# Kernel tuning notes

Measured on AMD Instinct MI355X. Metric: run time of the kernel, lower is better.

## Reference

```python
import jax, jax.numpy as jnp
import numpy as np

# Complete K-ary forest: B trees, depth D levels, BFS node numbering per tree.
B, K, D = 64, 4, 6
V, L = 600, 256
N_PER = (K ** D - 1) // (K - 1)   # 1365 nodes per tree
N = B * N_PER                      # 87360 total nodes


def _schedule():
    """Per-(depth, sibling_index) groups, mirroring the torch decode_train loop
    for a complete K-ary forest. Returns list of (d, s, node_idx, parent_idx)."""
    starts = [(K ** d - 1) // (K - 1) for d in range(D)]  # level offsets within a tree
    tree_off = np.arange(B)[:, None] * N_PER
    groups = []
    for d in range(D):
        for s in (range(1) if d == 0 else range(K)):
            if d == 0:
                p = np.arange(1)                      # root
                par = None
            else:
                p = np.arange(K ** (d - 1)) * K + s   # positions with sib_pos == s
                par = (tree_off + starts[d - 1] + (p // K)[None, :]).reshape(-1)
            idx = (tree_off + starts[d] + p[None, :]).reshape(-1)
            groups.append((d, s, jnp.asarray(idx),
                           None if par is None else jnp.asarray(par)))
    return groups

GROUPS = _schedule()


def _lstm(gx, h, c, W_hh, b_ih, b_hh):
    # torch LSTMCell, gate order i, f, g, o; gx = x @ W_ih^T precomputed.
    gates = gx + b_ih + h @ W_hh.T + b_hh
    i, f, g, o = jnp.split(gates, 4, axis=1)
    c_new = jax.nn.sigmoid(f) * c + jax.nn.sigmoid(i) * jnp.tanh(g)
    return jax.nn.sigmoid(o) * jnp.tanh(c_new), c_new


def setup_inputs() -> dict:
    key = jax.random.key(0)
    ks = jax.random.split(key, 20)
    w = lambda k, shape, s=0.05: jax.random.normal(k, shape, dtype=jnp.float32) * s
    return {
        'z': w(ks[0], (B, L), 1.0),
        'features': jax.random.randint(ks[1], (N,), 0, V),
        'W_ih_p': w(ks[2], (4 * L, V)), 'W_hh_p': w(ks[3], (4 * L, L)),
        'b_ih_p': w(ks[4], (4 * L,)), 'b_hh_p': w(ks[5], (4 * L,)),
        'W_ih_s': w(ks[6], (4 * L, V)), 'W_hh_s': w(ks[7], (4 * L, L)),
        'b_ih_s': w(ks[8], (4 * L,)), 'b_hh_s': w(ks[9], (4 * L,)),
        'U_parent': w(ks[10], (L, L)), 'U_sibling': w(ks[11], (L, L)),
        'W_label': w(ks[12], (V, L)), 'b_label': w(ks[13], (V,)),
        'W_depth': w(ks[14], (1, L)), 'b_depth': w(ks[15], (1,)),
        'W_width': w(ks[16], (1, L)), 'b_width': w(ks[17], (1,)),
        'w_off_p': w(ks[18], (1, 1), 1.0), 'w_off_s': w(ks[19], (1, 1), 1.0),
    }


def reference(z, features, W_ih_p, W_hh_p, b_ih_p, b_hh_p,
              W_ih_s, W_hh_s, b_ih_s, b_hh_s, U_parent, U_sibling,
              W_label, b_label, W_depth, b_depth, W_width, b_width,
              w_off_p, w_off_s):
    h_p = jnp.zeros((N, L), jnp.float32)
    c_p = jnp.zeros((N, L), jnp.float32)
    h_s = jnp.zeros((N, L), jnp.float32)
    c_s = jnp.zeros((N, L), jnp.float32)
    pred_labels = jnp.zeros((N, V), jnp.float32)
    pred_is_parent = jnp.zeros((N,), jnp.float32)
    pred_has_sib = jnp.zeros((N,), jnp.float32)

    for d, s, idx, pidx in GROUPS:
        G = idx.shape[0]
        if d == 0:
            h_par, c_par = z, jnp.zeros((B, L), jnp.float32)
        else:
            h_par, c_par = h_p[pidx], c_p[pidx]
        if s == 0:
            h_prev = jnp.zeros((G, L), jnp.float32)
            c_prev = jnp.zeros((G, L), jnp.float32)
        else:
            h_prev, c_prev = h_s[idx - 1], c_s[idx - 1]
        # group-constant teacher flags for a complete K-ary tree
        is_par = 1.0 if d < D - 1 else 0.0
        has_sib = 1.0 if (d > 0 and s < K - 1) else 0.0

        h_pred = jnp.tanh(h_par @ U_parent.T + h_prev @ U_sibling.T)
        logits = h_pred @ W_label.T + b_label
        p_par = jax.nn.sigmoid(h_pred @ W_depth.T + b_depth)[:, 0]
        p_sib = jax.nn.sigmoid(h_pred @ W_width.T + b_width)[:, 0]
        logp = jax.nn.log_softmax(
            logits + w_off_p[0, 0] * is_par + w_off_s[0, 0] * has_sib, axis=1)

        lab = features[idx]
        gx_p = jnp.take(W_ih_p, lab, axis=1).T  # one-hot @ W_ih^T as a gather
        gx_s = jnp.take(W_ih_s, lab, axis=1).T
        hp_new, cp_new = _lstm(gx_p, h_par, c_par, W_hh_p, b_ih_p, b_hh_p)
        hs_new, cs_new = _lstm(gx_s, h_prev, c_prev, W_hh_s, b_ih_s, b_hh_s)

        h_p = h_p.at[idx].set(hp_new)
        c_p = c_p.at[idx].set(cp_new)
        h_s = h_s.at[idx].set(hs_new)
        c_s = c_s.at[idx].set(cs_new)
        pred_labels = pred_labels.at[idx].set(logp)
        pred_is_parent = pred_is_parent.at[idx].set(p_par)
        pred_has_sib = pred_has_sib.at[idx].set(p_sib)

    # pack [N, V+2]: log-softmax labels, p(is_parent), p(has_sibling)
    return jnp.concatenate(
        [pred_labels, pred_is_parent[:, None], pred_has_sib[:, None]], axis=1)
```

## Files before the change

kernel.cpp:

```cpp
#include <hip/hip_runtime.h>


typedef unsigned short u16;
typedef short bf16x8 __attribute__((ext_vector_type(8)));
typedef float f32x4 __attribute__((ext_vector_type(4)));

#define NPER 1365
#define VDIM 600
#define VD2  602

#define MODE_PPA   0
#define MODE_UPROJ 1
#define MODE_ROOT  2

__device__ __forceinline__ float b2f(u16 h) {
  union { unsigned u; float f; } v; v.u = ((unsigned)h) << 16; return v.f;
}
__device__ __forceinline__ u16 f2bf(float f) {
  union { float f; unsigned u; } v; v.f = f;
  unsigned r = v.u + 0x7fff + ((v.u >> 16) & 1);
  return (u16)(r >> 16);
}
__device__ __forceinline__ float fsigm(float x) {
  return __fdividef(1.f, 1.f + __expf(-x));
}
__device__ __forceinline__ float ftanh(float x) {
  float e = __expf(-2.f * fabsf(x));
  float r = __fdividef(1.f - e, 1.f + e);
  return x < 0.f ? -r : r;
}

__device__ __forceinline__ void ladder(int r, int& off, int& pcs, int& start) {
  if (r < 64)        { off = 0;    pcs = 0; start = 1;   }
  else if (r < 320)  { off = 64;   pcs = 2; start = 5;   }
  else if (r < 1344) { off = 320;  pcs = 4; start = 21;  }
  else if (r < 5440) { off = 1344; pcs = 6; start = 85;  }
  else               { off = 5440; pcs = 8; start = 341; }
}

__global__ void k_pack(
    const float* __restrict__ Upar, const float* __restrict__ Whhp,
    const float* __restrict__ Usib, const float* __restrict__ Whhs,
    const float* __restrict__ z, const float* __restrict__ Wihp,
    const float* __restrict__ Wihs, const float* __restrict__ Wlab,
    const float* __restrict__ Wd, const float* __restrict__ Ww,
    const float* __restrict__ blab, const float* __restrict__ bd,
    const float* __restrict__ bw, const float* __restrict__ bihp,
    const float* __restrict__ bhhp, const float* __restrict__ bihs,
    const float* __restrict__ bhhs,
    u16* __restrict__ UPWHHP, u16* __restrict__ USWHHS, u16* __restrict__ ZBF,
    u16* __restrict__ WIHPT, u16* __restrict__ WIHST, u16* __restrict__ WEXT,
    float* __restrict__ BE, float* __restrict__ BP, float* __restrict__ BS) {
  int i = blockIdx.x * 256 + threadIdx.x;
  if (i < 327680) {
    int r = i >> 8, c = i & 255;
    UPWHHP[i] = f2bf(r < 256 ? Upar[(r << 8) | c] : Whhp[((r - 256) << 8) | c]);
    return;
  }
  i -= 327680;
  if (i < 327680) {
    int r = i >> 8, c = i & 255;
    USWHHS[i] = f2bf(r < 256 ? Usib[(r << 8) | c] : Whhs[((r - 256) << 8) | c]);
    return;
  }
  i -= 327680;
  if (i < 16384) { ZBF[i] = f2bf(z[i]); return; }
  i -= 16384;
  if (i < 614400) {
    int r = i >> 10, c = i & 1023;
    WIHPT[i] = f2bf(Wihp[c * VDIM + r]); return;
  }
  i -= 614400;
  if (i < 614400) {
    int r = i >> 10, c = i & 1023;
    WIHST[i] = f2bf(Wihs[c * VDIM + r]); return;
  }
  i -= 614400;
  if (i < VD2 * 256) {
    int r = i >> 8, c = i & 255;
    float v = (r < VDIM) ? Wlab[r * 256 + c] : ((r == VDIM) ? Wd[c] : Ww[c]);
    WEXT[i] = f2bf(v); return;
  }
  i -= VD2 * 256;
  if (i < VD2) { BE[i] = (i < VDIM) ? blab[i] : ((i == VDIM) ? bd[0] : bw[0]); return; }
  i -= VD2;
  if (i < 1024) { BP[i] = bihp[i] + bhhp[i]; return; }
  i -= 1024;
  if (i < 1024) { BS[i] = bihs[i] + bhhs[i]; return; }
}

__device__ __forceinline__ void dev_dual(
    int tile, int nx, const u16* __restrict__ A, const u16* __restrict__ B,
    int M, int mode, u16* __restrict__ ppa, int ppoff,
    float* __restrict__ uproj, u16* __restrict__ gates,
    u16* __restrict__ hroot) {
  static __shared__ __align__(16) u16 As[128 * 40];
  static __shared__ __align__(16) u16 Bs[128 * 40];
  const int m0 = (tile % nx) * 128, n0 = (tile / nx) * 128;
  const int tid = threadIdx.x;
  const int wave = tid >> 6, lane = tid & 63;
  const int quad = lane >> 4, lr = lane & 15;
  const int wm = (wave >> 1) * 64, wn = (wave & 1) * 64;
  const int srow = tid >> 2;
  const int sch = (tid & 3) << 3;

  f32x4 acc[4][4] = {};
  for (int t = 0; t < 8; ++t) {
    const int kk = t * 32;
    bf16x8 a0 = *(const bf16x8*)(A + (size_t)(m0 + srow) * 256 + kk + sch);
    bf16x8 a1 = *(const bf16x8*)(A + (size_t)(m0 + srow + 64) * 256 + kk + sch);
    bf16x8 b0 = *(const bf16x8*)(B + (size_t)(n0 + srow) * 256 + kk + sch);
    bf16x8 b1 = *(const bf16x8*)(B + (size_t)(n0 + srow + 64) * 256 + kk + sch);
    __syncthreads();
    *(bf16x8*)&As[srow * 40 + sch] = a0;
    *(bf16x8*)&As[(srow + 64) * 40 + sch] = a1;
    *(bf16x8*)&Bs[srow * 40 + sch] = b0;
    *(bf16x8*)&Bs[(srow + 64) * 40 + sch] = b1;
    __syncthreads();
    bf16x8 af[4], bfr[4];
#pragma unroll
    for (int tm = 0; tm < 4; ++tm)
      af[tm] = *(const bf16x8*)&As[(wm + tm * 16 + lr) * 40 + quad * 8];
#pragma unroll
    for (int tn = 0; tn < 4; ++tn)
      bfr[tn] = *(const bf16x8*)&Bs[(wn + tn * 16 + lr) * 40 + quad * 8];
#pragma unroll
    for (int tm = 0; tm < 4; ++tm)
#pragma unroll
      for (int tn = 0; tn < 4; ++tn)
        acc[tm][tn] = __builtin_amdgcn_mfma_f32_16x16x32_bf16(
            af[tm], bfr[tn], acc[tm][tn], 0, 0, 0);
  }

  const bool isg = (n0 >= 256);
#pragma unroll
  for (int tn = 0; tn < 4; ++tn) {
    int col = n0 + wn + tn * 16 + lr;
#pragma unroll
    for (int tm = 0; tm < 4; ++tm) {
#pragma unroll
      for (int r = 0; r < 4; ++r) {
        int row = m0 + wm + tm * 16 + quad * 4 + r;
        if (row >= M) continue;
        float v = acc[tm][tn][r];
        if (isg) {
          gates[(size_t)row * 1024 + (col - 256)] = f2bf(v);
        } else if (mode == MODE_PPA) {
          ppa[(size_t)(ppoff + row) * 256 + col] = f2bf(v);
        } else if (mode == MODE_UPROJ) {
          uproj[(size_t)row * 256 + col] = v;
        } else {
          hroot[(size_t)row * 256 + col] = f2bf(ftanh(v));
        }
      }
    }
  }
}


__device__ __forceinline__ void dev_s0(int r, const u16* __restrict__ wihT,
    const float* __restrict__ bias, const int* __restrict__ feat,
    u16* __restrict__ h, u16* __restrict__ c) {
  int u = threadIdx.x;
  int off, pcs, start; ladder(r, off, pcs, start);
  int lg = r - off;
  int t = lg >> pcs, j = lg & ((1 << pcs) - 1);
  int lab = feat[t * NPER + start + 4 * j];
  const u16* wr = wihT + lab * 1024;
  float gi = b2f(wr[u])       + bias[u];
  float gg = b2f(wr[512 + u]) + bias[512 + u];
  float go = b2f(wr[768 + u]) + bias[768 + u];
  float cn = fsigm(gi) * ftanh(gg);
  float hn = fsigm(go) * ftanh(cn);
  h[(size_t)r * 256 + u] = f2bf(hn);
  c[(size_t)r * 256 + u] = f2bf(cn);
}

__device__ __forceinline__ void dev_lstm_sib(int r, int k,
    const u16* __restrict__ gates, const u16* __restrict__ wihT,
    const float* __restrict__ bias, const u16* __restrict__ c_in,
    const int* __restrict__ feat, u16* __restrict__ h, u16* __restrict__ c) {
  int u = threadIdx.x;
  int off, pcs, start; ladder(r, off, pcs, start);
  int lg = r - off;
  int t = lg >> pcs, j = lg & ((1 << pcs) - 1);
  int lab = feat[t * NPER + start + 4 * j + k];
  const u16* wr = wihT + lab * 1024;
  const u16* gr = gates + (size_t)r * 1024;
  float gi = b2f(wr[u])       + bias[u]       + b2f(gr[u]);
  float gf = b2f(wr[256 + u]) + bias[256 + u] + b2f(gr[256 + u]);
  float gg = b2f(wr[512 + u]) + bias[512 + u] + b2f(gr[512 + u]);
  float go = b2f(wr[768 + u]) + bias[768 + u] + b2f(gr[768 + u]);
  float cv = b2f(c_in[(size_t)r * 256 + u]);
  float cn = fsigm(gf) * cv + fsigm(gi) * ftanh(gg);
  float hn = fsigm(go) * ftanh(cn);
  h[(size_t)r * 256 + u] = f2bf(hn);
  c[(size_t)r * 256 + u] = f2bf(cn);
}

__device__ __forceinline__ void dev_lstm_par(int g,
    const u16* __restrict__ gates, const u16* __restrict__ wihT,
    const float* __restrict__ bias, const u16* __restrict__ c_in,
    const int* __restrict__ feat, u16* __restrict__ h, u16* __restrict__ c,
    int lsbits, int start) {
  int u = threadIdx.x;
  int t = g >> lsbits, p = g & ((1 << lsbits) - 1);
  int pr = lsbits ? ((t << (lsbits - 2)) | (p >> 2)) : g;
  int lab = feat[t * NPER + start + p];
  const u16* wr = wihT + lab * 1024;
  const u16* gr = gates + (size_t)pr * 1024;
  float gi = b2f(wr[u])       + bias[u]       + b2f(gr[u]);
  float gf = b2f(wr[256 + u]) + bias[256 + u] + b2f(gr[256 + u]);
  float gg = b2f(wr[512 + u]) + bias[512 + u] + b2f(gr[512 + u]);
  float go = b2f(wr[768 + u]) + bias[768 + u] + b2f(gr[768 + u]);
  float cv = c_in ? b2f(c_in[(size_t)pr * 256 + u]) : 0.f;
  float cn = fsigm(gf) * cv + fsigm(gi) * ftanh(gg);
  float hn = fsigm(go) * ftanh(cn);
  h[(size_t)g * 256 + u] = f2bf(hn);
  c[(size_t)g * 256 + u] = f2bf(cn);
}


__global__ __launch_bounds__(256) void k_s0(
    const u16* WIHST, const float* BS, const int* feat, u16* h, u16* c) {
  dev_s0(blockIdx.x, WIHST, BS, feat, h, c);
}

__global__ __launch_bounds__(256) void k_gg(
    int nA,
    const u16* Aa, const u16* Ba, int Ma, int nxa, int modea,
    u16* ppaa, int ppoffa, float* uproja, u16* gatesa, u16* hroota,
    const u16* Ab, const u16* Bb, int Mb, int nxb, int modeb,
    u16* ppab, int ppoffb, float* uprojb, u16* gatesb, u16* hrootb) {
  int b = blockIdx.x;
  if (b < nA)
    dev_dual(b, nxa, Aa, Ba, Ma, modea, ppaa, ppoffa, uproja, gatesa, hroota);
  else
    dev_dual(b - nA, nxb, Ab, Bb, Mb, modeb, ppab, ppoffb, uprojb, gatesb,
             hrootb);
}

__global__ __launch_bounds__(256) void k_gemm(
    const u16* A, const u16* B, int M, int nx, int mode,
    u16* ppa, int ppoff, float* uproj, u16* gates, u16* hroot) {
  dev_dual(blockIdx.x, nx, A, B, M, mode, ppa, ppoff, uproj, gates, hroot);
}

__global__ __launch_bounds__(256) void k_ll(
    int nP,
    const u16* gatesP, const u16* WIHPT, const float* BP, const u16* cpin,
    u16* hpout, u16* cpout, int lsbits, int startp,
    int kS, const u16* gatesS, const u16* WIHST, const float* BS,
    const u16* csin, u16* hsout, u16* csout, const int* feat) {
  int b = blockIdx.x;
  if (b < nP)
    dev_lstm_par(b, gatesP, WIHPT, BP, cpin, feat, hpout, cpout, lsbits,
                 startp);
  else
    dev_lstm_sib(b - nP, kS, gatesS, WIHST, BS, csin, feat, hsout, csout);
}

__global__ __launch_bounds__(256) void k_plstm(
    const u16* gatesP, const u16* WIHPT, const float* BP, const u16* cpin,
    const int* feat, u16* hpout, u16* cpout, int lsbits, int start) {
  dev_lstm_par(blockIdx.x, gatesP, WIHPT, BP, cpin, feat, hpout, cpout,
               lsbits, start);
}

__global__ __launch_bounds__(256, 2) void k_tail32(
    const u16* __restrict__ HROOT, const u16* __restrict__ PPA,
    const float* __restrict__ U1, const float* __restrict__ U2,
    const float* __restrict__ U3, const u16* __restrict__ B,
    const float* __restrict__ bias, float* __restrict__ out) {
  __shared__ __align__(16) u16 As[32 * 264];
  __shared__ float smax[32][4], ssum[32][4], slz[32];
  const int m0 = blockIdx.x * 32;
  const int tid = threadIdx.x;
  const int wave = tid >> 6, lane = tid & 63;
  const int quad = lane >> 4, lr = lane & 15;
  const int c0 = wave * 160;

#pragma unroll
  for (int cch = 0; cch < 4; ++cch) {
    int idx = cch * 256 + tid;
    int row = idx >> 5, ch = (idx & 31) << 3;
    int node = m0 + row;
    int t = node / NPER;
    int q = node - t * NPER;
    bf16x8 v8;
    if (q == 0) {
      v8 = *(const bf16x8*)(HROOT + (size_t)t * 256 + ch);
    } else {
      int off, pcs, start;
      if (q < 5)        { off = 0;    pcs = 0; start = 1;   }
      else if (q < 21)  { off = 64;   pcs = 2; start = 5;   }
      else if (q < 85)  { off = 320;  pcs = 4; start = 21;  }
      else if (q < 341) { off = 1344; pcs = 6; start = 85;  }
      else              { off = 5440; pcs = 8; start = 341; }
      int qq = q - start;
      int s = qq & 3, j = qq >> 2;
      int r = off + (t << pcs) + j;
      size_t ro = (size_t)r * 256 + ch;
      bf16x8 pp = *(const bf16x8*)(PPA + ro);
      const float* Us = (s == 1) ? U1 : ((s == 2) ? U2 : U3);
#pragma unroll
      for (int e = 0; e < 8; ++e) {
        float v = b2f((u16)pp[e]);
        if (s) v += Us[ro + e];
        v8[e] = (short)f2bf(ftanh(v));
      }
    }
    *(bf16x8*)&As[row * 264 + ch] = v8;
  }
  __syncthreads();

  f32x4 acc[2][10] = {};
#pragma unroll
  for (int t = 0; t < 8; ++t) {
    bf16x8 af[2], bfr[10];
#pragma unroll
    for (int tm = 0; tm < 2; ++tm)
      af[tm] = *(const bf16x8*)&As[(tm * 16 + lr) * 264 + t * 32 + quad * 8];
#pragma unroll
    for (int tn = 0; tn < 10; ++tn)
      bfr[tn] = *(const bf16x8*)(B + (size_t)(c0 + tn * 16 + lr) * 256 +
                                 t * 32 + quad * 8);
#pragma unroll
    for (int tm = 0; tm < 2; ++tm)
#pragma unroll
      for (int tn = 0; tn < 10; ++tn)
        acc[tm][tn] = __builtin_amdgcn_mfma_f32_16x16x32_bf16(
            af[tm], bfr[tn], acc[tm][tn], 0, 0, 0);
  }

  float bv[10]; bool val[10];
#pragma unroll
  for (int tn = 0; tn < 10; ++tn) {
    int col = c0 + tn * 16 + lr;
    val[tn] = (col < VDIM);
    bv[tn] = (col < VD2) ? bias[col] : 0.f;
  }

#pragma unroll
  for (int tm = 0; tm < 2; ++tm) {
#pragma unroll
    for (int r = 0; r < 4; ++r) {
      float mx = -1e30f;
#pragma unroll
      for (int tn = 0; tn < 10; ++tn)
        if (val[tn]) mx = fmaxf(mx, acc[tm][tn][r] + bv[tn]);
#pragma unroll
      for (int o = 1; o < 16; o <<= 1) mx = fmaxf(mx, __shfl_xor(mx, o, 64));
      if (lr == 0) smax[tm * 16 + quad * 4 + r][wave] = mx;
    }
  }
  __syncthreads();
#pragma unroll
  for (int tm = 0; tm < 2; ++tm) {
#pragma unroll
    for (int r = 0; r < 4; ++r) {
      int row = tm * 16 + quad * 4 + r;
      float fm = fmaxf(fmaxf(smax[row][0], smax[row][1]),
                       fmaxf(smax[row][2], smax[row][3]));
      float se = 0.f;
#pragma unroll
      for (int tn = 0; tn < 10; ++tn)
        if (val[tn]) se += __expf(acc[tm][tn][r] + bv[tn] - fm);
#pragma unroll
      for (int o = 1; o < 16; o <<= 1) se += __shfl_xor(se, o, 64);
      if (lr == 0) ssum[row][wave] = se;
    }
  }
  __syncthreads();
  if (tid < 32) {
    float fm = fmaxf(fmaxf(smax[tid][0], smax[tid][1]),
                     fmaxf(smax[tid][2], smax[tid][3]));
    slz[tid] = fm + __logf(ssum[tid][0] + ssum[tid][1] +
                           ssum[tid][2] + ssum[tid][3]);
  }
  __syncthreads();

#pragma unroll
  for (int tm = 0; tm < 2; ++tm) {
#pragma unroll
    for (int tn = 0; tn < 10; ++tn) {
      int col = c0 + tn * 16 + lr;
      if (col >= VD2) continue;
#pragma unroll
      for (int r = 0; r < 4; ++r) {
        int row = tm * 16 + quad * 4 + r;
        float v = acc[tm][tn][r] + bv[tn];
        out[(size_t)(m0 + row) * VD2 + col] =
            (col < VDIM) ? (v - slz[row]) : fsigm(v);
      }
    }
  }
}


extern "C" void kernel_launch(void* const* d_in, const int* in_sizes, int n_in,
                              void* d_out, int out_size, void* d_ws, size_t ws_size,
                              hipStream_t stream) {
  const float* z    = (const float*)d_in[0];
  const int*   feat = (const int*)d_in[1];
  const float* Wihp = (const float*)d_in[2];
  const float* Whhp = (const float*)d_in[3];
  const float* bihp = (const float*)d_in[4];
  const float* bhhp = (const float*)d_in[5];
  const float* Wihs = (const float*)d_in[6];
  const float* Whhs = (const float*)d_in[7];
  const float* bihs = (const float*)d_in[8];
  const float* bhhs = (const float*)d_in[9];
  const float* Upar = (const float*)d_in[10];
  const float* Usib = (const float*)d_in[11];
  const float* Wlab = (const float*)d_in[12];
  const float* blab = (const float*)d_in[13];
  const float* Wd   = (const float*)d_in[14];
  const float* bd   = (const float*)d_in[15];
  const float* Ww   = (const float*)d_in[16];
  const float* bw   = (const float*)d_in[17];
  float* out = (float*)d_out;

  char* w = (char*)d_ws;
  auto alloc = [&](size_t bytes) {
    char* p = w; w += (bytes + 255) & ~(size_t)255; return p;
  };
  u16*   UPWHHP = (u16*)alloc((size_t)1280 * 256 * 2);
  u16*   USWHHS = (u16*)alloc((size_t)1280 * 256 * 2);
  u16*   ZBF    = (u16*)alloc((size_t)128 * 256 * 2);
  u16*   WIHPT  = (u16*)alloc((size_t)VDIM * 1024 * 2);
  u16*   WIHST  = (u16*)alloc((size_t)VDIM * 1024 * 2);
  u16*   WEXT   = (u16*)alloc((size_t)640 * 256 * 2);
  float* BE     = (float*)alloc(VD2 * 4);
  float* BP     = (float*)alloc(1024 * 4);
  float* BS     = (float*)alloc(1024 * 4);
  const size_t CR = 21888;
  u16*   HSA[3], *CSA[3];
  for (int k = 0; k < 3; ++k) {
    HSA[k] = (u16*)alloc(CR * 256 * 2);
    CSA[k] = (u16*)alloc(CR * 256 * 2);
  }
  float* UPROJ[3];
  for (int k = 0; k < 3; ++k) UPROJ[k] = (float*)alloc(CR * 256 * 4);
  u16*   PPA   = (u16*)alloc(CR * 256 * 2);
  u16*   HROOT = (u16*)alloc((size_t)64 * 256 * 2);
  const size_t SB = (size_t)16384 * 256 * 2;
  u16* HP[2] = {(u16*)alloc(SB), (u16*)alloc(SB)};
  u16* CP[2] = {(u16*)alloc(SB), (u16*)alloc(SB)};
  u16*   GATES  = (u16*)alloc(CR * 1024 * 2);
  u16*   GATESP = (u16*)alloc((size_t)4096 * 1024 * 2);

  k_pack<<<8037, 256, 0, stream>>>(Upar, Whhp, Usib, Whhs, z, Wihp, Wihs,
                                   Wlab, Wd, Ww, blab, bd, bw, bihp, bhhp,
                                   bihs, bhhs, UPWHHP, USWHHS, ZBF, WIHPT,
                                   WIHST, WEXT, BE, BP, BS);
  k_s0<<<21824, 256, 0, stream>>>(WIHST, BS, feat, HSA[0], CSA[0]);
  k_gg<<<10 + 1710, 256, 0, stream>>>(
      10,
      ZBF, UPWHHP, 64, 1, MODE_ROOT, nullptr, 0, nullptr, GATESP, HROOT,
      HSA[0], USWHHS, 21824, 171, MODE_UPROJ, nullptr, 0, UPROJ[0], GATES,
      nullptr);
  k_ll<<<64 + 21824, 256, 0, stream>>>(
      64, GATESP, WIHPT, BP, nullptr, HP[0], CP[0], 0, 0,
      1, GATES, WIHST, BS, CSA[0], HSA[1], CSA[1], feat);
  k_gg<<<10 + 1710, 256, 0, stream>>>(
      10,
      HP[0], UPWHHP, 64, 1, MODE_PPA, PPA, 0, nullptr, GATESP, nullptr,
      HSA[1], USWHHS, 21824, 171, MODE_UPROJ, nullptr, 0, UPROJ[1], GATES,
      nullptr);
  k_ll<<<256 + 21824, 256, 0, stream>>>(
      256, GATESP, WIHPT, BP, CP[0], HP[1], CP[1], 2, 1,
      2, GATES, WIHST, BS, CSA[1], HSA[2], CSA[2], feat);
  k_gg<<<20 + 342, 256, 0, stream>>>(
      20,
      HP[1], UPWHHP, 256, 2, MODE_PPA, PPA, 64, nullptr, GATESP, nullptr,
      HSA[2], USWHHS, 21824, 171, MODE_UPROJ, nullptr, 0, UPROJ[2], nullptr,
      nullptr);
  k_plstm<<<1024, 256, 0, stream>>>(GATESP, WIHPT, BP, CP[1], feat,
                                    HP[0], CP[0], 4, 5);
  k_gemm<<<80, 256, 0, stream>>>(HP[0], UPWHHP, 1024, 8, MODE_PPA,
                                 PPA, 320, nullptr, GATESP, nullptr);
  k_plstm<<<4096, 256, 0, stream>>>(GATESP, WIHPT, BP, CP[0], feat,
                                    HP[1], CP[1], 6, 21);
  k_gemm<<<320, 256, 0, stream>>>(HP[1], UPWHHP, 4096, 32, MODE_PPA,
                                  PPA, 1344, nullptr, GATESP, nullptr);
  k_plstm<<<16384, 256, 0, stream>>>(GATESP, WIHPT, BP, CP[1], feat,
                                     HP[0], CP[0], 8, 85);
  k_gemm<<<256, 256, 0, stream>>>(HP[0], UPWHHP, 16384, 128, MODE_PPA,
                                  PPA, 5440, nullptr, nullptr, nullptr);
  k_tail32<<<2730, 256, 0, stream>>>(HROOT, PPA, UPROJ[0], UPROJ[1], UPROJ[2],
                                     WEXT, BE, out);

  (void)in_sizes; (void)n_in; (void)out_size; (void)ws_size;
}
```

Before: 657.4 us.

## Materialize h_pred in a separate assemble pass overlapped with last LSTM level

Moves the tanh(parent_proj + sibling_proj) assembly out of the tail GEMM's A-tile load into a dedicated HPRED buffer. Rows for shallower levels are assembled inside the final parent-LSTM launch as extra blocks, and the deepest level gets its own kernel after the last GEMM. The root hidden state is written straight into HPRED. The tail kernel then does plain contiguous loads of A, with no per-row ladder decode or gather. In exchange it adds a large extra bf16 buffer, a full write and read pass through memory, and one more kernel launch.

```diff
diff --git a/kernel.cpp b/kernel.cpp
--- a/kernel.cpp
+++ b/kernel.cpp
@@ -93,7 +93,7 @@
     int tile, int nx, const u16* __restrict__ A, const u16* __restrict__ B,
     int M, int mode, u16* __restrict__ ppa, int ppoff,
     float* __restrict__ uproj, u16* __restrict__ gates,
-    u16* __restrict__ hroot) {
+    u16* __restrict__ hpred) {
   static __shared__ __align__(16) u16 As[128 * 40];
   static __shared__ __align__(16) u16 Bs[128 * 40];
   const int m0 = (tile % nx) * 128, n0 = (tile / nx) * 128;
@@ -150,7 +150,7 @@
         } else if (mode == MODE_UPROJ) {
           uproj[(size_t)row * 256 + col] = v;
         } else {
-          hroot[(size_t)row * 256 + col] = f2bf(ftanh(v));
+          hpred[(size_t)row * NPER * 256 + col] = f2bf(ftanh(v));
         }
       }
     }
@@ -220,6 +220,23 @@
   c[(size_t)g * 256 + u] = f2bf(cn);
 }
 
+__device__ __forceinline__ void dev_assemble(int r,
+    const u16* __restrict__ PPA, const float* __restrict__ U1,
+    const float* __restrict__ U2, const float* __restrict__ U3,
+    u16* __restrict__ HPRED) {
+  int u = threadIdx.x;
+  int off, pcs, start; ladder(r, off, pcs, start);
+  int lg = r - off;
+  int t = lg >> pcs, j = lg & ((1 << pcs) - 1);
+  size_t base = ((size_t)(t * NPER + start + 4 * j)) * 256 + u;
+  size_t ro = (size_t)r * 256 + u;
+  float pp = b2f(PPA[ro]);
+  HPRED[base]       = f2bf(ftanh(pp));
+  HPRED[base + 256] = f2bf(ftanh(pp + U1[ro]));
+  HPRED[base + 512] = f2bf(ftanh(pp + U2[ro]));
+  HPRED[base + 768] = f2bf(ftanh(pp + U3[ro]));
+}
+
 
 __global__ __launch_bounds__(256) void k_s0(
     const u16* WIHST, const float* BS, const int* feat, u16* h, u16* c) {
@@ -229,21 +246,21 @@
 __global__ __launch_bounds__(256) void k_gg(
     int nA,
     const u16* Aa, const u16* Ba, int Ma, int nxa, int modea,
-    u16* ppaa, int ppoffa, float* uproja, u16* gatesa, u16* hroota,
+    u16* ppaa, int ppoffa, float* uproja, u16* gatesa, u16* hpreda,
     const u16* Ab, const u16* Bb, int Mb, int nxb, int modeb,
-    u16* ppab, int ppoffb, float* uprojb, u16* gatesb, u16* hrootb) {
+    u16* ppab, int ppoffb, float* uprojb, u16* gatesb, u16* hpredb) {
   int b = blockIdx.x;
   if (b < nA)
-    dev_dual(b, nxa, Aa, Ba, Ma, modea, ppaa, ppoffa, uproja, gatesa, hroota);
+    dev_dual(b, nxa, Aa, Ba, Ma, modea, ppaa, ppoffa, uproja, gatesa, hpreda);
   else
     dev_dual(b - nA, nxb, Ab, Bb, Mb, modeb, ppab, ppoffb, uprojb, gatesb,
-             hrootb);
+             hpredb);
 }
 
 __global__ __launch_bounds__(256) void k_gemm(
     const u16* A, const u16* B, int M, int nx, int mode,
-    u16* ppa, int ppoff, float* uproj, u16* gates, u16* hroot) {
-  dev_dual(blockIdx.x, nx, A, B, M, mode, ppa, ppoff, uproj, gates, hroot);
+    u16* ppa, int ppoff, float* uproj, u16* gates, u16* hpred) {
+  dev_dual(blockIdx.x, nx, A, B, M, mode, ppa, ppoff, uproj, gates, hpred);
 }
 
 __global__ __launch_bounds__(256) void k_ll(
@@ -267,10 +284,26 @@
                lsbits, start);
 }
 
-__global__ __launch_bounds__(256, 2) void k_tail32(
-    const u16* __restrict__ HROOT, const u16* __restrict__ PPA,
-    const float* __restrict__ U1, const float* __restrict__ U2,
-    const float* __restrict__ U3, const u16* __restrict__ B,
+__global__ __launch_bounds__(256) void k_plstm_asm(
+    const u16* gatesP, const u16* WIHPT, const float* BP, const u16* cpin,
+    const int* feat, u16* hpout, u16* cpout,
+    const u16* PPA, const float* U1, const float* U2, const float* U3,
+    u16* HPRED) {
+  int b = blockIdx.x;
+  if (b < 16384)
+    dev_lstm_par(b, gatesP, WIHPT, BP, cpin, feat, hpout, cpout, 8, 85);
+  else
+    dev_assemble(b - 16384, PPA, U1, U2, U3, HPRED);
+}
+
+__global__ __launch_bounds__(256) void k_assemble(
+    const u16* PPA, const float* U1, const float* U2, const float* U3,
+    u16* HPRED) {
+  dev_assemble(5440 + blockIdx.x, PPA, U1, U2, U3, HPRED);
+}
+
+__global__ __launch_bounds__(256, 2) void k_mm_tail(
+    const u16* __restrict__ A, const u16* __restrict__ B,
     const float* __restrict__ bias, float* __restrict__ out) {
   __shared__ __align__(16) u16 As[32 * 264];
   __shared__ float smax[32][4], ssum[32][4], slz[32];
@@ -281,36 +314,11 @@
   const int c0 = wave * 160;
 
 #pragma unroll
-  for (int cch = 0; cch < 4; ++cch) {
-    int idx = cch * 256 + tid;
+  for (int c = 0; c < 4; ++c) {
+    int idx = c * 256 + tid;
     int row = idx >> 5, ch = (idx & 31) << 3;
-    int node = m0 + row;
-    int t = node / NPER;
-    int q = node - t * NPER;
-    bf16x8 v8;
-    if (q == 0) {
-      v8 = *(const bf16x8*)(HROOT + (size_t)t * 256 + ch);
-    } else {
-      int off, pcs, start;
-      if (q < 5)        { off = 0;    pcs = 0; start = 1;   }
-      else if (q < 21)  { off = 64;   pcs = 2; start = 5;   }
-      else if (q < 85)  { off = 320;  pcs = 4; start = 21;  }
-      else if (q < 341) { off = 1344; pcs = 6; start = 85;  }
-      else              { off = 5440; pcs = 8; start = 341; }
-      int qq = q - start;
-      int s = qq & 3, j = qq >> 2;
-      int r = off + (t << pcs) + j;
-      size_t ro = (size_t)r * 256 + ch;
-      bf16x8 pp = *(const bf16x8*)(PPA + ro);
-      const float* Us = (s == 1) ? U1 : ((s == 2) ? U2 : U3);
-#pragma unroll
-      for (int e = 0; e < 8; ++e) {
-        float v = b2f((u16)pp[e]);
-        if (s) v += Us[ro + e];
-        v8[e] = (short)f2bf(ftanh(v));
-      }
-    }
-    *(bf16x8*)&As[row * 264 + ch] = v8;
+    *(bf16x8*)&As[row * 264 + ch] =
+        *(const bf16x8*)(A + (size_t)(m0 + row) * 256 + ch);
   }
   __syncthreads();
 
@@ -443,12 +451,12 @@
   float* UPROJ[3];
   for (int k = 0; k < 3; ++k) UPROJ[k] = (float*)alloc(CR * 256 * 4);
   u16*   PPA   = (u16*)alloc(CR * 256 * 2);
-  u16*   HROOT = (u16*)alloc((size_t)64 * 256 * 2);
   const size_t SB = (size_t)16384 * 256 * 2;
   u16* HP[2] = {(u16*)alloc(SB), (u16*)alloc(SB)};
   u16* CP[2] = {(u16*)alloc(SB), (u16*)alloc(SB)};
   u16*   GATES  = (u16*)alloc(CR * 1024 * 2);
   u16*   GATESP = (u16*)alloc((size_t)4096 * 1024 * 2);
+  u16*   HPRED  = (u16*)alloc((size_t)87424 * 256 * 2);
 
   k_pack<<<8037, 256, 0, stream>>>(Upar, Whhp, Usib, Whhs, z, Wihp, Wihs,
                                    Wlab, Wd, Ww, blab, bd, bw, bihp, bhhp,
@@ -457,7 +465,7 @@
   k_s0<<<21824, 256, 0, stream>>>(WIHST, BS, feat, HSA[0], CSA[0]);
   k_gg<<<10 + 1710, 256, 0, stream>>>(
       10,
-      ZBF, UPWHHP, 64, 1, MODE_ROOT, nullptr, 0, nullptr, GATESP, HROOT,
+      ZBF, UPWHHP, 64, 1, MODE_ROOT, nullptr, 0, nullptr, GATESP, HPRED,
       HSA[0], USWHHS, 21824, 171, MODE_UPROJ, nullptr, 0, UPROJ[0], GATES,
       nullptr);
   k_ll<<<64 + 21824, 256, 0, stream>>>(
@@ -484,12 +492,14 @@
                                     HP[1], CP[1], 6, 21);
   k_gemm<<<320, 256, 0, stream>>>(HP[1], UPWHHP, 4096, 32, MODE_PPA,
                                   PPA, 1344, nullptr, GATESP, nullptr);
-  k_plstm<<<16384, 256, 0, stream>>>(GATESP, WIHPT, BP, CP[1], feat,
-                                     HP[0], CP[0], 8, 85);
+  k_plstm_asm<<<16384 + 5440, 256, 0, stream>>>(
+      GATESP, WIHPT, BP, CP[1], feat, HP[0], CP[0],
+      PPA, UPROJ[0], UPROJ[1], UPROJ[2], HPRED);
   k_gemm<<<256, 256, 0, stream>>>(HP[0], UPWHHP, 16384, 128, MODE_PPA,
                                   PPA, 5440, nullptr, nullptr, nullptr);
-  k_tail32<<<2730, 256, 0, stream>>>(HROOT, PPA, UPROJ[0], UPROJ[1], UPROJ[2],
-                                     WEXT, BE, out);
+  k_assemble<<<16384, 256, 0, stream>>>(PPA, UPROJ[0], UPROJ[1], UPROJ[2],
+                                        HPRED);
+  k_mm_tail<<<2730, 256, 0, stream>>>(HPRED, WEXT, BE, out);
 
   (void)in_sizes; (void)n_in; (void)out_size; (void)ws_size;
 }
```

New measurement: 620.0 us. 1.06x faster.
